# Kernel tuning notes

Hardware: AMD Instinct MI355X
Metric: run time of the kernel (lower is better)

The kernel has to match this reference:

```python
import jax, jax.numpy as jnp
import numpy as np

HEADS = 16
D_MODEL = 1024
GROUP = 4
SEQ = 2048
HEAD_DIM = D_MODEL // HEADS          # 64
KV_HEADS = HEADS // GROUP            # 4


def rope_tables(head_dim, seq_len, base=10000.0):
    # NOTE: faithful to source: exp = -2*arange(0,d,2)/d  (steps of 2 -> base^{-4j/d})
    exp = -2.0 * jnp.arange(0, head_dim, 2, dtype=jnp.float32) / head_dim
    thetas = jnp.power(base, exp)                       # [d/2]
    m = jnp.arange(seq_len, dtype=jnp.float32)          # [S]
    freq = jnp.outer(m, thetas)                         # [S, d/2]
    return jnp.cos(freq), jnp.sin(freq)


def apply_rope(x, cos, sin):
    # x: [B,S,H,D]; complex rotation on consecutive pairs
    B, S, H, D = x.shape
    xr = x.reshape(B, S, H, D // 2, 2)
    x0, x1 = xr[..., 0], xr[..., 1]
    c = cos[None, :S, None, :]
    s = sin[None, :S, None, :]
    out = jnp.stack([x0 * c - x1 * s, x0 * s + x1 * c], axis=-1)
    return out.reshape(B, S, H, D)


def setup_inputs() -> dict:
    key = jax.random.key(0)
    ks = jax.random.split(key, 8)
    B = 1
    q = jax.random.normal(ks[0], (B, SEQ, D_MODEL), dtype=jnp.float32)
    k = jax.random.normal(ks[1], (B, SEQ, D_MODEL), dtype=jnp.float32)
    v = jax.random.normal(ks[2], (B, SEQ, D_MODEL), dtype=jnp.float32)
    mask = jnp.tril(jnp.ones((SEQ, SEQ), dtype=jnp.int32))[None]  # causal [B,S,S]
    sc = 0.02
    Wq = jax.random.normal(ks[3], (D_MODEL, D_MODEL), dtype=jnp.float32) * sc
    Wk = jax.random.normal(ks[4], (D_MODEL, D_MODEL // GROUP), dtype=jnp.float32) * sc
    Wv = jax.random.normal(ks[5], (D_MODEL, D_MODEL // GROUP), dtype=jnp.float32) * sc
    Wo = jax.random.normal(ks[6], (D_MODEL, D_MODEL), dtype=jnp.float32) * sc
    bq = jnp.zeros((D_MODEL,), jnp.float32)
    bk = jnp.zeros((D_MODEL // GROUP,), jnp.float32)
    bv = jnp.zeros((D_MODEL // GROUP,), jnp.float32)
    bo = jnp.zeros((D_MODEL,), jnp.float32)
    return {"q": q, "k": k, "v": v, "mask": mask, "Wq": Wq, "bq": bq,
            "Wk": Wk, "bk": bk, "Wv": Wv, "bv": bv, "Wo": Wo, "bo": bo}


def reference(q, k, v, mask, Wq, bq, Wk, bk, Wv, bv, Wo, bo):
    B, S, _ = q.shape
    cos, sin = rope_tables(HEAD_DIM, S)
    qh = (q @ Wq + bq).reshape(B, S, HEADS, HEAD_DIM)
    kh = (k @ Wk + bk).reshape(B, S, KV_HEADS, HEAD_DIM)
    vh = (v @ Wv + bv).reshape(B, S, KV_HEADS, HEAD_DIM)
    qh = apply_rope(qh, cos, sin)
    kh = apply_rope(kh, cos, sin)
    qh = qh.transpose(0, 2, 1, 3)                       # [B,H,S,D]
    kh = kh.transpose(0, 2, 1, 3)                       # [B,Hkv,S,D]
    vh = vh.transpose(0, 2, 1, 3)
    # torch .repeat tiles: query head j attends kv head j % KV_HEADS
    kh = jnp.tile(kh, (1, GROUP, 1, 1))                 # [B,H,S,D]
    vh = jnp.tile(vh, (1, GROUP, 1, 1))
    scores = jnp.einsum('bhqd,bhkd->bhqk', qh, kh) / jnp.sqrt(
        jnp.asarray(HEAD_DIM, dtype=qh.dtype))
    scores = jnp.where(mask[:, None, :, :] == 0, -jnp.inf, scores)
    attn = jax.nn.softmax(scores, axis=-1)
    out = jnp.einsum('bhqk,bhkd->bhqd', attn, vh)
    out = out.transpose(0, 2, 1, 3).reshape(B, S, D_MODEL)
    return out @ Wo + bo
```

## Files before the change

kernel.cpp:

```cpp
#include <hip/hip_runtime.h>
#include <hip/hip_bf16.h>
#include <math.h>


#define SEQ 2048
#define DM 1024
#define HD 64

using u16 = unsigned short;
typedef __attribute__((ext_vector_type(8))) short bf16x8;
typedef __attribute__((ext_vector_type(4))) float f32x4;

#define QSCALE 0.18033688011112042f

__device__ __forceinline__ u16 f2b(float f) {
    union { float f; unsigned int i; } v; v.f = f;
    unsigned int u = v.i;
    return (u16)((u + 0x7fffu + ((u >> 16) & 1u)) >> 16);
}
__device__ __forceinline__ u16 f2b_fast(float f) {
    union { float f; unsigned int i; } v; v.f = f;
    return (u16)((v.i + 0x8000u) >> 16);
}

__global__ __launch_bounds__(256) void prep_kernel(
    const float* __restrict__ qin, const float* __restrict__ kin, const float* __restrict__ vin,
    const float* __restrict__ Wq, const float* __restrict__ Wk,
    const float* __restrict__ Wv, const float* __restrict__ Wo,
    u16* __restrict__ Xq, u16* __restrict__ Xk, u16* __restrict__ Xv,
    u16* __restrict__ Wt, u16* __restrict__ wot)
{
    const int b = blockIdx.x;
    const int t = threadIdx.x;

    if (b < 640) {
        __shared__ short T[64][72];
        const float* W; u16* dst; int N, t0, rowoff;
        if (b < 256)      { W = Wq; dst = Wt;  N = 1024; t0 = b;       rowoff = 0; }
        else if (b < 320) { W = Wk; dst = Wt;  N = 256;  t0 = b - 256; rowoff = 1024; }
        else if (b < 384) { W = Wv; dst = Wt;  N = 256;  t0 = b - 320; rowoff = 1280; }
        else              { W = Wo; dst = wot; N = 1024; t0 = b - 384; rowoff = 0; }
        const int ntn = N >> 6;
        const int k0 = (t0 / ntn) * 64, n0 = (t0 % ntn) * 64;
        const int r = t >> 4, c4 = (t & 15) * 4;
        #pragma unroll
        for (int rr = 0; rr < 4; ++rr) {
            const int k = r + rr * 16;
            float4 w4 = *reinterpret_cast<const float4*>(W + (size_t)(k0 + k) * N + n0 + c4);
            T[c4 + 0][k] = (short)f2b(w4.x);
            T[c4 + 1][k] = (short)f2b(w4.y);
            T[c4 + 2][k] = (short)f2b(w4.z);
            T[c4 + 3][k] = (short)f2b(w4.w);
        }
        __syncthreads();
        const int n = t >> 2, ck = (t & 3) * 16;
        u16* dp = dst + (size_t)(rowoff + n0 + n) * DM + k0 + ck;
        *reinterpret_cast<bf16x8*>(dp)     = *reinterpret_cast<const bf16x8*>(&T[n][ck]);
        *reinterpret_cast<bf16x8*>(dp + 8) = *reinterpret_cast<const bf16x8*>(&T[n][ck + 8]);
    } else {
        const int idx = b - 640;
        const int which = idx >> 8;
        const int ib = idx & 255;
        const float* src = (which == 0) ? qin : (which == 1) ? kin : vin;
        u16* dst = (which == 0) ? Xq : (which == 1) ? Xk : Xv;
        const size_t base = (size_t)ib * 8192 + (size_t)t * 32;
        #pragma unroll
        for (int c = 0; c < 4; ++c) {
            float4 x0 = *reinterpret_cast<const float4*>(src + base + c * 8);
            float4 x1 = *reinterpret_cast<const float4*>(src + base + c * 8 + 4);
            bf16x8 o;
            o[0] = (short)f2b(x0.x); o[1] = (short)f2b(x0.y);
            o[2] = (short)f2b(x0.z); o[3] = (short)f2b(x0.w);
            o[4] = (short)f2b(x1.x); o[5] = (short)f2b(x1.y);
            o[6] = (short)f2b(x1.z); o[7] = (short)f2b(x1.w);
            *reinterpret_cast<bf16x8*>(dst + base + c * 8) = o;
        }
    }
}

__global__ __launch_bounds__(256) void proj_mfma(
    const u16* __restrict__ Xq, const u16* __restrict__ Xk, const u16* __restrict__ Xv,
    const u16* __restrict__ Wt,
    const float* __restrict__ bq, const float* __restrict__ bk, const float* __restrict__ bv,
    u16* __restrict__ Qr, u16* __restrict__ Kr, u16* __restrict__ Vrt)
{
    const int n0 = blockIdx.x * 64, m0 = blockIdx.y * 64;
    const int zone = (n0 < 1024) ? 0 : (n0 < 1280) ? 1 : 2;
    const u16* __restrict__ Az = (zone == 0) ? Xq : (zone == 1) ? Xk : Xv;

    __shared__ short As[64][72];
    __shared__ short Bs[64][72];

    const int t = threadIdx.x;
    const int w = t >> 6, lane = t & 63, lm = lane & 15, quad = lane >> 4;
    const int sr = t >> 2, sc = (t & 3) * 16;

    f32x4 acc[4] = { {0,0,0,0}, {0,0,0,0}, {0,0,0,0}, {0,0,0,0} };

    for (int k0 = 0; k0 < DM; k0 += 64) {
        const u16* ap = Az + (size_t)(m0 + sr) * DM + k0 + sc;
        *reinterpret_cast<bf16x8*>(&As[sr][sc])     = *reinterpret_cast<const bf16x8*>(ap);
        *reinterpret_cast<bf16x8*>(&As[sr][sc + 8]) = *reinterpret_cast<const bf16x8*>(ap + 8);
        const u16* bp = Wt + (size_t)(n0 + sr) * DM + k0 + sc;
        *reinterpret_cast<bf16x8*>(&Bs[sr][sc])     = *reinterpret_cast<const bf16x8*>(bp);
        *reinterpret_cast<bf16x8*>(&Bs[sr][sc + 8]) = *reinterpret_cast<const bf16x8*>(bp + 8);
        __syncthreads();
        bf16x8 af0 = *reinterpret_cast<const bf16x8*>(&As[16 * w + lm][quad * 8]);
        bf16x8 af1 = *reinterpret_cast<const bf16x8*>(&As[16 * w + lm][32 + quad * 8]);
        #pragma unroll
        for (int nb = 0; nb < 4; ++nb) {
            bf16x8 b0 = *reinterpret_cast<const bf16x8*>(&Bs[16 * nb + lm][quad * 8]);
            bf16x8 b1 = *reinterpret_cast<const bf16x8*>(&Bs[16 * nb + lm][32 + quad * 8]);
            acc[nb] = __builtin_amdgcn_mfma_f32_16x16x32_bf16(af0, b0, acc[nb], 0, 0, 0);
            acc[nb] = __builtin_amdgcn_mfma_f32_16x16x32_bf16(af1, b1, acc[nb], 0, 0, 0);
        }
        __syncthreads();
    }

    const float* __restrict__ bias = (zone == 0) ? bq : (zone == 1) ? bk : bv;
    const int nbase = (zone == 0) ? n0 : (zone == 1) ? (n0 - 1024) : (n0 - 1280);
    const int head = nbase >> 6;
    #pragma unroll
    for (int nb = 0; nb < 4; ++nb) {
        const int d = 16 * nb + lm;
        const float bvv = bias[nbase + d];
        float vals[4];
        #pragma unroll
        for (int r = 0; r < 4; ++r) vals[r] = acc[nb][r] + bvv;
        if (zone != 2) {
            const int pi = d >> 1;
            const float theta = exp2f(-0.8304820237f * (float)pi);
            const bool odd = (lm & 1);
            const float sca = (zone == 0) ? QSCALE : 1.0f;
            #pragma unroll
            for (int r = 0; r < 4; ++r) {
                const int m = m0 + 16 * w + quad * 4 + r;
                float sn, cs;
                sincosf((float)m * theta, &sn, &cs);
                float x  = vals[r];
                float xp = __shfl_xor(x, 1);
                vals[r] = (odd ? (xp * sn + x * cs) : (x * cs - xp * sn)) * sca;
            }
            u16* op = (zone == 0 ? Qr : Kr) + (size_t)head * SEQ * HD;
            #pragma unroll
            for (int r = 0; r < 4; ++r) {
                const int m = m0 + 16 * w + quad * 4 + r;
                op[(size_t)m * HD + d] = f2b(vals[r]);
            }
        } else {
            u16 pk[4];
            #pragma unroll
            for (int r = 0; r < 4; ++r) pk[r] = f2b(vals[r]);
            u16* vp = Vrt + ((size_t)head * HD + d) * SEQ + m0 + 16 * w + quad * 4;
            *reinterpret_cast<uint2*>(vp) = *reinterpret_cast<uint2*>(pk);
        }
    }
}

__global__ __launch_bounds__(256) void attn_mfma(
    const u16* __restrict__ Qr, const u16* __restrict__ Kr, const u16* __restrict__ Vrt,
    u16* __restrict__ AO)
{
    const int h  = blockIdx.x;
    const int qy = blockIdx.y;
    const int qt = (qy < 16) ? (2 * qy) : (63 - 2 * qy);
    const int kvh = h & 3;

    __shared__ short Qs[64][72];
    __shared__ short Ks[2][64][72];
    __shared__ short Vt[64][136];
    __shared__ short Ps[64][136];
    __shared__ float Lred[4][64];

    const int t = threadIdx.x;
    const int w = t >> 6, lane = t & 63, lm = lane & 15, quad = lane >> 4;
    const int sr = t >> 2, sc = (t & 3) * 16;
    const int colb = (sc >> 4) * 32;

    {
        const u16* qp = Qr + ((size_t)h * SEQ + qt * 64 + sr) * HD + sc;
        *reinterpret_cast<bf16x8*>(&Qs[sr][sc])     = *reinterpret_cast<const bf16x8*>(qp);
        *reinterpret_cast<bf16x8*>(&Qs[sr][sc + 8]) = *reinterpret_cast<const bf16x8*>(qp + 8);
    }
    __syncthreads();
    bf16x8 bq[4][2];
    #pragma unroll
    for (int nb = 0; nb < 4; ++nb) {
        bq[nb][0] = *reinterpret_cast<const bf16x8*>(&Qs[16 * nb + lm][quad * 8]);
        bq[nb][1] = *reinterpret_cast<const bf16x8*>(&Qs[16 * nb + lm][32 + quad * 8]);
    }

    f32x4 O[4][4];
    #pragma unroll
    for (int i = 0; i < 4; ++i)
        #pragma unroll
        for (int j = 0; j < 4; ++j) O[i][j] = (f32x4){0.f, 0.f, 0.f, 0.f};
    float lp[4] = { 0.f, 0.f, 0.f, 0.f };

    const int ntile = qt + 1;
    const u16* kbase = Kr  + ((size_t)kvh * SEQ + sr) * HD + sc;
    const u16* vbase = Vrt + ((size_t)kvh * HD  + sr) * SEQ + sc;

    for (int u = 0; u < ntile; u += 2) {
        const bool has1 = (u + 1 < ntile);
        {
            const u16* kp0 = kbase + (size_t)u * 64 * HD;
            *reinterpret_cast<bf16x8*>(&Ks[0][sr][sc])     = *reinterpret_cast<const bf16x8*>(kp0);
            *reinterpret_cast<bf16x8*>(&Ks[0][sr][sc + 8]) = *reinterpret_cast<const bf16x8*>(kp0 + 8);
            const u16* vp0 = vbase + (size_t)u * 64;
            *reinterpret_cast<bf16x8*>(&Vt[sr][colb])      = *reinterpret_cast<const bf16x8*>(vp0);
            *reinterpret_cast<bf16x8*>(&Vt[sr][colb + 8])  = *reinterpret_cast<const bf16x8*>(vp0 + 8);
            if (has1) {
                const u16* kp1 = kbase + (size_t)(u + 1) * 64 * HD;
                *reinterpret_cast<bf16x8*>(&Ks[1][sr][sc])     = *reinterpret_cast<const bf16x8*>(kp1);
                *reinterpret_cast<bf16x8*>(&Ks[1][sr][sc + 8]) = *reinterpret_cast<const bf16x8*>(kp1 + 8);
                const u16* vp1 = vbase + (size_t)(u + 1) * 64;
                *reinterpret_cast<bf16x8*>(&Vt[sr][colb + 16]) = *reinterpret_cast<const bf16x8*>(vp1);
                *reinterpret_cast<bf16x8*>(&Vt[sr][colb + 24]) = *reinterpret_cast<const bf16x8*>(vp1 + 8);
            } else {
                bf16x8 z = {0,0,0,0,0,0,0,0};
                *reinterpret_cast<bf16x8*>(&Vt[sr][colb + 16]) = z;
                *reinterpret_cast<bf16x8*>(&Vt[sr][colb + 24]) = z;
            }
        }
        __syncthreads();

        #pragma unroll
        for (int tp = 0; tp < 2; ++tp) {
            const int kt = u + tp;
            if (tp == 1 && !has1) {
                const uint2 z2 = make_uint2(0u, 0u);
                #pragma unroll
                for (int nb = 0; nb < 4; ++nb)
                    *reinterpret_cast<uint2*>(&Ps[16 * nb + lm][w * 32 + 16 + quad * 4]) = z2;
                continue;
            }
            const bf16x8 ak0 = *reinterpret_cast<const bf16x8*>(&Ks[tp][16 * w + lm][quad * 8]);
            const bf16x8 ak1 = *reinterpret_cast<const bf16x8*>(&Ks[tp][16 * w + lm][32 + quad * 8]);
            const bool diag = (kt == qt);
            #pragma unroll
            for (int nb = 0; nb < 4; ++nb) {
                f32x4 ss = { 0.f, 0.f, 0.f, 0.f };
                ss = __builtin_amdgcn_mfma_f32_16x16x32_bf16(ak0, bq[nb][0], ss, 0, 0, 0);
                ss = __builtin_amdgcn_mfma_f32_16x16x32_bf16(ak1, bq[nb][1], ss, 0, 0, 0);
                u16 pk[4];
                #pragma unroll
                for (int r = 0; r < 4; ++r) {
                    float sv = ss[r];
                    if (diag && (16 * w + quad * 4 + r > 16 * nb + lm)) sv = -INFINITY;
                    float e = __builtin_amdgcn_exp2f(fminf(sv, 126.f));
                    lp[nb] += e;
                    pk[r] = f2b_fast(e);
                }
                *reinterpret_cast<uint2*>(&Ps[16 * nb + lm][w * 32 + tp * 16 + quad * 4]) =
                    *reinterpret_cast<uint2*>(pk);
            }
        }

        #pragma unroll
        for (int db = 0; db < 4; ++db) {
            const bf16x8 av = *reinterpret_cast<const bf16x8*>(&Vt[16 * db + lm][w * 32 + quad * 8]);
            #pragma unroll
            for (int nb = 0; nb < 4; ++nb) {
                const bf16x8 bp = *reinterpret_cast<const bf16x8*>(&Ps[16 * nb + lm][w * 32 + quad * 8]);
                O[db][nb] = __builtin_amdgcn_mfma_f32_16x16x32_bf16(av, bp, O[db][nb], 0, 0, 0);
            }
        }
        __syncthreads();
    }

    #pragma unroll
    for (int nb = 0; nb < 4; ++nb) {
        lp[nb] += __shfl_xor(lp[nb], 16);
        lp[nb] += __shfl_xor(lp[nb], 32);
    }
    if (quad == 0) {
        #pragma unroll
        for (int nb = 0; nb < 4; ++nb) Lred[w][16 * nb + lm] = lp[nb];
    }

    float* Sf = reinterpret_cast<float*>(&Ps[0][0]);
    #pragma unroll
    for (int ph = 0; ph < 4; ++ph) {
        __syncthreads();
        if (w == ph) {
            #pragma unroll
            for (int db = 0; db < 4; ++db)
                #pragma unroll
                for (int nb = 0; nb < 4; ++nb)
                    #pragma unroll
                    for (int r = 0; r < 4; ++r) {
                        const int d = 16 * db + quad * 4 + r, q = 16 * nb + lm;
                        const float v = O[db][nb][r];
                        Sf[q * 68 + d] = (ph == 0) ? v : (Sf[q * 68 + d] + v);
                    }
        }
    }
    __syncthreads();

    {
        const int q = t >> 2, dc = (t & 3) * 16;
        const float linv = 1.0f / (Lred[0][q] + Lred[1][q] + Lred[2][q] + Lred[3][q]);
        u16 pk[16];
        #pragma unroll
        for (int j = 0; j < 16; ++j)
            pk[j] = f2b(Sf[q * 68 + dc + j] * linv);
        u16* op = AO + (size_t)(qt * 64 + q) * DM + h * HD + dc;
        *reinterpret_cast<bf16x8*>(op)     = *reinterpret_cast<const bf16x8*>(pk);
        *reinterpret_cast<bf16x8*>(op + 8) = *reinterpret_cast<const bf16x8*>(pk + 8);
    }
}

__global__ __launch_bounds__(256) void oproj_mfma(
    const u16* __restrict__ AO, const u16* __restrict__ wot,
    const float* __restrict__ bo, float* __restrict__ out)
{
    __shared__ short As[64][72];
    __shared__ short Bs[64][72];
    const int t = threadIdx.x;
    const int w = t >> 6, lane = t & 63, lm = lane & 15, quad = lane >> 4;
    const int m0 = blockIdx.y * 64, n0 = blockIdx.x * 64;
    const int sr = t >> 2, sc = (t & 3) * 16;

    f32x4 acc[4] = { {0,0,0,0}, {0,0,0,0}, {0,0,0,0}, {0,0,0,0} };

    for (int k0 = 0; k0 < DM; k0 += 64) {
        const u16* ap = AO + (size_t)(m0 + sr) * DM + k0 + sc;
        *reinterpret_cast<bf16x8*>(&As[sr][sc])     = *reinterpret_cast<const bf16x8*>(ap);
        *reinterpret_cast<bf16x8*>(&As[sr][sc + 8]) = *reinterpret_cast<const bf16x8*>(ap + 8);
        const u16* bp = wot + (size_t)(n0 + sr) * DM + k0 + sc;
        *reinterpret_cast<bf16x8*>(&Bs[sr][sc])     = *reinterpret_cast<const bf16x8*>(bp);
        *reinterpret_cast<bf16x8*>(&Bs[sr][sc + 8]) = *reinterpret_cast<const bf16x8*>(bp + 8);
        __syncthreads();
        bf16x8 af0 = *reinterpret_cast<const bf16x8*>(&As[16 * w + lm][quad * 8]);
        bf16x8 af1 = *reinterpret_cast<const bf16x8*>(&As[16 * w + lm][32 + quad * 8]);
        #pragma unroll
        for (int nb = 0; nb < 4; ++nb) {
            bf16x8 b0 = *reinterpret_cast<const bf16x8*>(&Bs[16 * nb + lm][quad * 8]);
            bf16x8 b1 = *reinterpret_cast<const bf16x8*>(&Bs[16 * nb + lm][32 + quad * 8]);
            acc[nb] = __builtin_amdgcn_mfma_f32_16x16x32_bf16(af0, b0, acc[nb], 0, 0, 0);
            acc[nb] = __builtin_amdgcn_mfma_f32_16x16x32_bf16(af1, b1, acc[nb], 0, 0, 0);
        }
        __syncthreads();
    }

    #pragma unroll
    for (int nb = 0; nb < 4; ++nb) {
        const int dl = 16 * nb + lm;
        const float bv = bo[n0 + dl];
        #pragma unroll
        for (int r = 0; r < 4; ++r) {
            const int m = m0 + 16 * w + quad * 4 + r;
            out[(size_t)m * DM + n0 + dl] = acc[nb][r] + bv;
        }
    }
}

extern "C" void kernel_launch(void* const* d_in, const int* in_sizes, int n_in,
                              void* d_out, int out_size, void* d_ws, size_t ws_size,
                              hipStream_t stream)
{
    const float* q  = (const float*)d_in[0];
    const float* k  = (const float*)d_in[1];
    const float* v  = (const float*)d_in[2];
    const float* Wq = (const float*)d_in[4];
    const float* bq = (const float*)d_in[5];
    const float* Wk = (const float*)d_in[6];
    const float* bk = (const float*)d_in[7];
    const float* Wv = (const float*)d_in[8];
    const float* bv = (const float*)d_in[9];
    const float* Wo = (const float*)d_in[10];
    const float* bo = (const float*)d_in[11];
    float* out = (float*)d_out;

    u16* Xq  = (u16*)d_ws;
    u16* Xk  = Xq  + (size_t)SEQ * DM;
    u16* Xv  = Xk  + (size_t)SEQ * DM;
    u16* Wt  = Xv  + (size_t)SEQ * DM;
    u16* wot = Wt  + (size_t)1536 * 1024;
    u16* Qr  = wot + (size_t)1024 * 1024;
    u16* Kr  = Qr  + (size_t)16 * SEQ * HD;
    u16* Vrt = Kr  + (size_t)4 * SEQ * HD;
    u16* AO  = Vrt + (size_t)4 * SEQ * HD;

    hipLaunchKernelGGL(prep_kernel, dim3(1408), dim3(256), 0, stream,
                       q, k, v, Wq, Wk, Wv, Wo, Xq, Xk, Xv, Wt, wot);
    hipLaunchKernelGGL(proj_mfma, dim3(24, 32), dim3(256), 0, stream,
                       Xq, Xk, Xv, Wt, bq, bk, bv, Qr, Kr, Vrt);
    hipLaunchKernelGGL(attn_mfma, dim3(16, 32), dim3(256), 0, stream,
                       Qr, Kr, Vrt, AO);
    hipLaunchKernelGGL(oproj_mfma, dim3(16, 32), dim3(256), 0, stream,
                       AO, wot, bo, out);
}
```

Baseline: 184.0 us.

## Replace LDS-tiled GEMMs and attention with register-direct per-wave MFMA loads

```diff
diff --git a/kernel.cpp b/kernel.cpp
--- a/kernel.cpp
+++ b/kernel.cpp
@@ -84,77 +84,92 @@
     const float* __restrict__ bq, const float* __restrict__ bk, const float* __restrict__ bv,
     u16* __restrict__ Qr, u16* __restrict__ Kr, u16* __restrict__ Vrt)
 {
-    const int n0 = blockIdx.x * 64, m0 = blockIdx.y * 64;
+    const int t = threadIdx.x;
+    const int w = t >> 6, lane = t & 63, lm = lane & 15, quad = lane >> 4;
+    const int n0 = blockIdx.x * 64 + (w & 1) * 32;
+    const int m0 = blockIdx.y * 64 + (w >> 1) * 32;
     const int zone = (n0 < 1024) ? 0 : (n0 < 1280) ? 1 : 2;
     const u16* __restrict__ Az = (zone == 0) ? Xq : (zone == 1) ? Xk : Xv;
 
-    __shared__ short As[64][72];
-    __shared__ short Bs[64][72];
-
-    const int t = threadIdx.x;
-    const int w = t >> 6, lane = t & 63, lm = lane & 15, quad = lane >> 4;
-    const int sr = t >> 2, sc = (t & 3) * 16;
-
-    f32x4 acc[4] = { {0,0,0,0}, {0,0,0,0}, {0,0,0,0}, {0,0,0,0} };
-
-    for (int k0 = 0; k0 < DM; k0 += 64) {
-        const u16* ap = Az + (size_t)(m0 + sr) * DM + k0 + sc;
-        *reinterpret_cast<bf16x8*>(&As[sr][sc])     = *reinterpret_cast<const bf16x8*>(ap);
-        *reinterpret_cast<bf16x8*>(&As[sr][sc + 8]) = *reinterpret_cast<const bf16x8*>(ap + 8);
-        const u16* bp = Wt + (size_t)(n0 + sr) * DM + k0 + sc;
-        *reinterpret_cast<bf16x8*>(&Bs[sr][sc])     = *reinterpret_cast<const bf16x8*>(bp);
-        *reinterpret_cast<bf16x8*>(&Bs[sr][sc + 8]) = *reinterpret_cast<const bf16x8*>(bp + 8);
-        __syncthreads();
-        bf16x8 af0 = *reinterpret_cast<const bf16x8*>(&As[16 * w + lm][quad * 8]);
-        bf16x8 af1 = *reinterpret_cast<const bf16x8*>(&As[16 * w + lm][32 + quad * 8]);
-        #pragma unroll
-        for (int nb = 0; nb < 4; ++nb) {
-            bf16x8 b0 = *reinterpret_cast<const bf16x8*>(&Bs[16 * nb + lm][quad * 8]);
-            bf16x8 b1 = *reinterpret_cast<const bf16x8*>(&Bs[16 * nb + lm][32 + quad * 8]);
-            acc[nb] = __builtin_amdgcn_mfma_f32_16x16x32_bf16(af0, b0, acc[nb], 0, 0, 0);
-            acc[nb] = __builtin_amdgcn_mfma_f32_16x16x32_bf16(af1, b1, acc[nb], 0, 0, 0);
-        }
-        __syncthreads();
+    const u16* arow[2] = { Az + (size_t)(m0 + lm) * DM + quad * 8,
+                           Az + (size_t)(m0 + 16 + lm) * DM + quad * 8 };
+    const u16* brow[2] = { Wt + (size_t)(n0 + lm) * DM + quad * 8,
+                           Wt + (size_t)(n0 + 16 + lm) * DM + quad * 8 };
+
+    f32x4 acc[2][2];
+    #pragma unroll
+    for (int i = 0; i < 2; ++i)
+        #pragma unroll
+        for (int j = 0; j < 2; ++j) acc[i][j] = (f32x4){0.f, 0.f, 0.f, 0.f};
+
+    bf16x8 a0[2], b0[2], a1[2], b1[2];
+    #pragma unroll
+    for (int i = 0; i < 2; ++i) {
+        a0[i] = *reinterpret_cast<const bf16x8*>(arow[i]);
+        b0[i] = *reinterpret_cast<const bf16x8*>(brow[i]);
+    }
+    for (int k = 0; k < DM; k += 64) {
+        #pragma unroll
+        for (int i = 0; i < 2; ++i) {
+            a1[i] = *reinterpret_cast<const bf16x8*>(arow[i] + k + 32);
+            b1[i] = *reinterpret_cast<const bf16x8*>(brow[i] + k + 32);
+        }
+        #pragma unroll
+        for (int mi = 0; mi < 2; ++mi)
+            #pragma unroll
+            for (int ni = 0; ni < 2; ++ni)
+                acc[mi][ni] = __builtin_amdgcn_mfma_f32_16x16x32_bf16(a0[mi], b0[ni], acc[mi][ni], 0, 0, 0);
+        if (k + 64 < DM) {
+            #pragma unroll
+            for (int i = 0; i < 2; ++i) {
+                a0[i] = *reinterpret_cast<const bf16x8*>(arow[i] + k + 64);
+                b0[i] = *reinterpret_cast<const bf16x8*>(brow[i] + k + 64);
+            }
+        }
+        #pragma unroll
+        for (int mi = 0; mi < 2; ++mi)
+            #pragma unroll
+            for (int ni = 0; ni < 2; ++ni)
+                acc[mi][ni] = __builtin_amdgcn_mfma_f32_16x16x32_bf16(a1[mi], b1[ni], acc[mi][ni], 0, 0, 0);
     }
 
     const float* __restrict__ bias = (zone == 0) ? bq : (zone == 1) ? bk : bv;
-    const int nbase = (zone == 0) ? n0 : (zone == 1) ? (n0 - 1024) : (n0 - 1280);
-    const int head = nbase >> 6;
-    #pragma unroll
-    for (int nb = 0; nb < 4; ++nb) {
-        const int d = 16 * nb + lm;
-        const float bvv = bias[nbase + d];
-        float vals[4];
-        #pragma unroll
-        for (int r = 0; r < 4; ++r) vals[r] = acc[nb][r] + bvv;
-        if (zone != 2) {
-            const int pi = d >> 1;
-            const float theta = exp2f(-0.8304820237f * (float)pi);
-            const bool odd = (lm & 1);
-            const float sca = (zone == 0) ? QSCALE : 1.0f;
-            #pragma unroll
-            for (int r = 0; r < 4; ++r) {
-                const int m = m0 + 16 * w + quad * 4 + r;
-                float sn, cs;
-                sincosf((float)m * theta, &sn, &cs);
-                float x  = vals[r];
-                float xp = __shfl_xor(x, 1);
-                vals[r] = (odd ? (xp * sn + x * cs) : (x * cs - xp * sn)) * sca;
-            }
-            u16* op = (zone == 0 ? Qr : Kr) + (size_t)head * SEQ * HD;
-            #pragma unroll
-            for (int r = 0; r < 4; ++r) {
-                const int m = m0 + 16 * w + quad * 4 + r;
-                op[(size_t)m * HD + d] = f2b(vals[r]);
-            }
-        } else {
-            u16 pk[4];
-            #pragma unroll
-            for (int r = 0; r < 4; ++r) pk[r] = f2b(vals[r]);
-            u16* vp = Vrt + ((size_t)head * HD + d) * SEQ + m0 + 16 * w + quad * 4;
-            *reinterpret_cast<uint2*>(vp) = *reinterpret_cast<uint2*>(pk);
-        }
-    }
+    const int zoff = (zone == 0) ? 0 : (zone == 1) ? 1024 : 1280;
+    #pragma unroll
+    for (int mi = 0; mi < 2; ++mi)
+        #pragma unroll
+        for (int ni = 0; ni < 2; ++ni) {
+            const int zc = (n0 - zoff) + ni * 16 + lm;
+            const int head = zc >> 6, d = zc & 63;
+            const float bvv = bias[zc];
+            float vals[4];
+            #pragma unroll
+            for (int r = 0; r < 4; ++r) vals[r] = acc[mi][ni][r] + bvv;
+            if (zone != 2) {
+                const int pi = d >> 1;
+                const float theta = exp2f(-0.8304820237f * (float)pi);
+                const bool odd = (lm & 1);
+                const float sca = (zone == 0) ? QSCALE : 1.0f;
+                u16* op = (zone == 0 ? Qr : Kr) + (size_t)head * SEQ * HD;
+                #pragma unroll
+                for (int r = 0; r < 4; ++r) {
+                    const int m = m0 + mi * 16 + quad * 4 + r;
+                    float sn, cs;
+                    sincosf((float)m * theta, &sn, &cs);
+                    float x  = vals[r];
+                    float xp = __shfl_xor(x, 1);
+                    float o  = (odd ? (xp * sn + x * cs) : (x * cs - xp * sn)) * sca;
+                    op[(size_t)m * HD + d] = f2b(o);
+                }
+            } else {
+                u16 pk[4];
+                #pragma unroll
+                for (int r = 0; r < 4; ++r) pk[r] = f2b(vals[r]);
+                const int m = m0 + mi * 16 + quad * 4;
+                u16* vp = Vrt + ((size_t)head * HD + d) * SEQ + m;
+                *reinterpret_cast<uint2*>(vp) = *reinterpret_cast<uint2*>(pk);
+            }
+        }
 }
 
 __global__ __launch_bounds__(256) void attn_mfma(
@@ -166,148 +181,83 @@
     const int qt = (qy < 16) ? (2 * qy) : (63 - 2 * qy);
     const int kvh = h & 3;
 
-    __shared__ short Qs[64][72];
-    __shared__ short Ks[2][64][72];
-    __shared__ short Vt[64][136];
-    __shared__ short Ps[64][136];
-    __shared__ float Lred[4][64];
+    __shared__ u16 Ps[4][16][76];
 
     const int t = threadIdx.x;
     const int w = t >> 6, lane = t & 63, lm = lane & 15, quad = lane >> 4;
-    const int sr = t >> 2, sc = (t & 3) * 16;
-    const int colb = (sc >> 4) * 32;
-
-    {
-        const u16* qp = Qr + ((size_t)h * SEQ + qt * 64 + sr) * HD + sc;
-        *reinterpret_cast<bf16x8*>(&Qs[sr][sc])     = *reinterpret_cast<const bf16x8*>(qp);
-        *reinterpret_cast<bf16x8*>(&Qs[sr][sc + 8]) = *reinterpret_cast<const bf16x8*>(qp + 8);
-    }
-    __syncthreads();
-    bf16x8 bq[4][2];
-    #pragma unroll
-    for (int nb = 0; nb < 4; ++nb) {
-        bq[nb][0] = *reinterpret_cast<const bf16x8*>(&Qs[16 * nb + lm][quad * 8]);
-        bq[nb][1] = *reinterpret_cast<const bf16x8*>(&Qs[16 * nb + lm][32 + quad * 8]);
-    }
-
-    f32x4 O[4][4];
-    #pragma unroll
-    for (int i = 0; i < 4; ++i)
-        #pragma unroll
-        for (int j = 0; j < 4; ++j) O[i][j] = (f32x4){0.f, 0.f, 0.f, 0.f};
+
+    const u16* qp = Qr + ((size_t)h * SEQ + qt * 64 + 16 * w + lm) * HD + quad * 8;
+    const bf16x8 aq0 = *reinterpret_cast<const bf16x8*>(qp);
+    const bf16x8 aq1 = *reinterpret_cast<const bf16x8*>(qp + 32);
+
+    const u16* krow = Kr  + ((size_t)kvh * SEQ + lm) * HD + quad * 8;
+    const u16* vrow = Vrt + ((size_t)kvh * HD + lm) * SEQ + quad * 8;
+
+    f32x4 O[4] = { {0,0,0,0}, {0,0,0,0}, {0,0,0,0}, {0,0,0,0} };
     float lp[4] = { 0.f, 0.f, 0.f, 0.f };
 
-    const int ntile = qt + 1;
-    const u16* kbase = Kr  + ((size_t)kvh * SEQ + sr) * HD + sc;
-    const u16* vbase = Vrt + ((size_t)kvh * HD  + sr) * SEQ + sc;
-
-    for (int u = 0; u < ntile; u += 2) {
-        const bool has1 = (u + 1 < ntile);
-        {
-            const u16* kp0 = kbase + (size_t)u * 64 * HD;
-            *reinterpret_cast<bf16x8*>(&Ks[0][sr][sc])     = *reinterpret_cast<const bf16x8*>(kp0);
-            *reinterpret_cast<bf16x8*>(&Ks[0][sr][sc + 8]) = *reinterpret_cast<const bf16x8*>(kp0 + 8);
-            const u16* vp0 = vbase + (size_t)u * 64;
-            *reinterpret_cast<bf16x8*>(&Vt[sr][colb])      = *reinterpret_cast<const bf16x8*>(vp0);
-            *reinterpret_cast<bf16x8*>(&Vt[sr][colb + 8])  = *reinterpret_cast<const bf16x8*>(vp0 + 8);
-            if (has1) {
-                const u16* kp1 = kbase + (size_t)(u + 1) * 64 * HD;
-                *reinterpret_cast<bf16x8*>(&Ks[1][sr][sc])     = *reinterpret_cast<const bf16x8*>(kp1);
-                *reinterpret_cast<bf16x8*>(&Ks[1][sr][sc + 8]) = *reinterpret_cast<const bf16x8*>(kp1 + 8);
-                const u16* vp1 = vbase + (size_t)(u + 1) * 64;
-                *reinterpret_cast<bf16x8*>(&Vt[sr][colb + 16]) = *reinterpret_cast<const bf16x8*>(vp1);
-                *reinterpret_cast<bf16x8*>(&Vt[sr][colb + 24]) = *reinterpret_cast<const bf16x8*>(vp1 + 8);
-            } else {
-                bf16x8 z = {0,0,0,0,0,0,0,0};
-                *reinterpret_cast<bf16x8*>(&Vt[sr][colb + 16]) = z;
-                *reinterpret_cast<bf16x8*>(&Vt[sr][colb + 24]) = z;
-            }
-        }
-        __syncthreads();
-
-        #pragma unroll
-        for (int tp = 0; tp < 2; ++tp) {
-            const int kt = u + tp;
-            if (tp == 1 && !has1) {
-                const uint2 z2 = make_uint2(0u, 0u);
+    u16* ps = &Ps[w][0][0];
+
+    for (int kt = 0; kt <= qt; ++kt) {
+        const int kb = kt * 64;
+        bf16x8 kb0[4], kb1[4], vb0[4], vb1[4];
+        #pragma unroll
+        for (int nb = 0; nb < 4; ++nb) {
+            const u16* kp = krow + (size_t)(kb + 16 * nb) * HD;
+            kb0[nb] = *reinterpret_cast<const bf16x8*>(kp);
+            kb1[nb] = *reinterpret_cast<const bf16x8*>(kp + 32);
+        }
+        #pragma unroll
+        for (int db = 0; db < 4; ++db) {
+            const u16* vp = vrow + (size_t)(16 * db) * SEQ + kb;
+            vb0[db] = *reinterpret_cast<const bf16x8*>(vp);
+            vb1[db] = *reinterpret_cast<const bf16x8*>(vp + 32);
+        }
+
+        f32x4 s[4];
+        #pragma unroll
+        for (int nb = 0; nb < 4; ++nb) {
+            f32x4 zz = { 0.f, 0.f, 0.f, 0.f };
+            zz = __builtin_amdgcn_mfma_f32_16x16x32_bf16(aq0, kb0[nb], zz, 0, 0, 0);
+            s[nb] = __builtin_amdgcn_mfma_f32_16x16x32_bf16(aq1, kb1[nb], zz, 0, 0, 0);
+        }
+
+        if (kt == qt) {
+            #pragma unroll
+            for (int nb = 0; nb < 4; ++nb)
                 #pragma unroll
-                for (int nb = 0; nb < 4; ++nb)
-                    *reinterpret_cast<uint2*>(&Ps[16 * nb + lm][w * 32 + 16 + quad * 4]) = z2;
-                continue;
-            }
-            const bf16x8 ak0 = *reinterpret_cast<const bf16x8*>(&Ks[tp][16 * w + lm][quad * 8]);
-            const bf16x8 ak1 = *reinterpret_cast<const bf16x8*>(&Ks[tp][16 * w + lm][32 + quad * 8]);
-            const bool diag = (kt == qt);
-            #pragma unroll
-            for (int nb = 0; nb < 4; ++nb) {
-                f32x4 ss = { 0.f, 0.f, 0.f, 0.f };
-                ss = __builtin_amdgcn_mfma_f32_16x16x32_bf16(ak0, bq[nb][0], ss, 0, 0, 0);
-                ss = __builtin_amdgcn_mfma_f32_16x16x32_bf16(ak1, bq[nb][1], ss, 0, 0, 0);
-                u16 pk[4];
-                #pragma unroll
-                for (int r = 0; r < 4; ++r) {
-                    float sv = ss[r];
-                    if (diag && (16 * w + quad * 4 + r > 16 * nb + lm)) sv = -INFINITY;
-                    float e = __builtin_amdgcn_exp2f(fminf(sv, 126.f));
-                    lp[nb] += e;
-                    pk[r] = f2b_fast(e);
-                }
-                *reinterpret_cast<uint2*>(&Ps[16 * nb + lm][w * 32 + tp * 16 + quad * 4]) =
-                    *reinterpret_cast<uint2*>(pk);
-            }
-        }
-
+                for (int r = 0; r < 4; ++r)
+                    if (16 * nb + lm > 16 * w + quad * 4 + r) s[nb][r] = -INFINITY;
+        }
+
+        #pragma unroll
+        for (int nb = 0; nb < 4; ++nb)
+            #pragma unroll
+            for (int r = 0; r < 4; ++r) {
+                float e = __builtin_amdgcn_exp2f(fminf(s[nb][r], 126.f));
+                lp[r] += e;
+                ps[(quad * 4 + r) * 76 + 16 * nb + lm] = f2b_fast(e);
+            }
+
+        const bf16x8 ap0 = *reinterpret_cast<const bf16x8*>(&ps[lm * 76 + quad * 8]);
+        const bf16x8 ap1 = *reinterpret_cast<const bf16x8*>(&ps[lm * 76 + 32 + quad * 8]);
         #pragma unroll
         for (int db = 0; db < 4; ++db) {
-            const bf16x8 av = *reinterpret_cast<const bf16x8*>(&Vt[16 * db + lm][w * 32 + quad * 8]);
-            #pragma unroll
-            for (int nb = 0; nb < 4; ++nb) {
-                const bf16x8 bp = *reinterpret_cast<const bf16x8*>(&Ps[16 * nb + lm][w * 32 + quad * 8]);
-                O[db][nb] = __builtin_amdgcn_mfma_f32_16x16x32_bf16(av, bp, O[db][nb], 0, 0, 0);
-            }
-        }
-        __syncthreads();
-    }
-
-    #pragma unroll
-    for (int nb = 0; nb < 4; ++nb) {
-        lp[nb] += __shfl_xor(lp[nb], 16);
-        lp[nb] += __shfl_xor(lp[nb], 32);
-    }
-    if (quad == 0) {
-        #pragma unroll
-        for (int nb = 0; nb < 4; ++nb) Lred[w][16 * nb + lm] = lp[nb];
-    }
-
-    float* Sf = reinterpret_cast<float*>(&Ps[0][0]);
-    #pragma unroll
-    for (int ph = 0; ph < 4; ++ph) {
-        __syncthreads();
-        if (w == ph) {
-            #pragma unroll
-            for (int db = 0; db < 4; ++db)
-                #pragma unroll
-                for (int nb = 0; nb < 4; ++nb)
-                    #pragma unroll
-                    for (int r = 0; r < 4; ++r) {
-                        const int d = 16 * db + quad * 4 + r, q = 16 * nb + lm;
-                        const float v = O[db][nb][r];
-                        Sf[q * 68 + d] = (ph == 0) ? v : (Sf[q * 68 + d] + v);
-                    }
-        }
-    }
-    __syncthreads();
-
-    {
-        const int q = t >> 2, dc = (t & 3) * 16;
-        const float linv = 1.0f / (Lred[0][q] + Lred[1][q] + Lred[2][q] + Lred[3][q]);
-        u16 pk[16];
-        #pragma unroll
-        for (int j = 0; j < 16; ++j)
-            pk[j] = f2b(Sf[q * 68 + dc + j] * linv);
-        u16* op = AO + (size_t)(qt * 64 + q) * DM + h * HD + dc;
-        *reinterpret_cast<bf16x8*>(op)     = *reinterpret_cast<const bf16x8*>(pk);
-        *reinterpret_cast<bf16x8*>(op + 8) = *reinterpret_cast<const bf16x8*>(pk + 8);
+            O[db] = __builtin_amdgcn_mfma_f32_16x16x32_bf16(ap0, vb0[db], O[db], 0, 0, 0);
+            O[db] = __builtin_amdgcn_mfma_f32_16x16x32_bf16(ap1, vb1[db], O[db], 0, 0, 0);
+        }
+    }
+
+    #pragma unroll
+    for (int r = 0; r < 4; ++r) {
+        #pragma unroll
+        for (int off = 1; off < 16; off <<= 1)
+            lp[r] += __shfl_xor(lp[r], off);
+        const float inv = 1.0f / lp[r];
+        const size_t row = (size_t)(qt * 64 + 16 * w + quad * 4 + r) * DM + (size_t)h * HD;
+        #pragma unroll
+        for (int db = 0; db < 4; ++db)
+            AO[row + 16 * db + lm] = f2b(O[db][r] * inv);
     }
 }
 
@@ -315,45 +265,65 @@
     const u16* __restrict__ AO, const u16* __restrict__ wot,
     const float* __restrict__ bo, float* __restrict__ out)
 {
-    __shared__ short As[64][72];
-    __shared__ short Bs[64][72];
     const int t = threadIdx.x;
     const int w = t >> 6, lane = t & 63, lm = lane & 15, quad = lane >> 4;
-    const int m0 = blockIdx.y * 64, n0 = blockIdx.x * 64;
-    const int sr = t >> 2, sc = (t & 3) * 16;
-
-    f32x4 acc[4] = { {0,0,0,0}, {0,0,0,0}, {0,0,0,0}, {0,0,0,0} };
-
-    for (int k0 = 0; k0 < DM; k0 += 64) {
-        const u16* ap = AO + (size_t)(m0 + sr) * DM + k0 + sc;
-        *reinterpret_cast<bf16x8*>(&As[sr][sc])     = *reinterpret_cast<const bf16x8*>(ap);
-        *reinterpret_cast<bf16x8*>(&As[sr][sc + 8]) = *reinterpret_cast<const bf16x8*>(ap + 8);
-        const u16* bp = wot + (size_t)(n0 + sr) * DM + k0 + sc;
-        *reinterpret_cast<bf16x8*>(&Bs[sr][sc])     = *reinterpret_cast<const bf16x8*>(bp);
-        *reinterpret_cast<bf16x8*>(&Bs[sr][sc + 8]) = *reinterpret_cast<const bf16x8*>(bp + 8);
-        __syncthreads();
-        bf16x8 af0 = *reinterpret_cast<const bf16x8*>(&As[16 * w + lm][quad * 8]);
-        bf16x8 af1 = *reinterpret_cast<const bf16x8*>(&As[16 * w + lm][32 + quad * 8]);
-        #pragma unroll
-        for (int nb = 0; nb < 4; ++nb) {
-            bf16x8 b0 = *reinterpret_cast<const bf16x8*>(&Bs[16 * nb + lm][quad * 8]);
-            bf16x8 b1 = *reinterpret_cast<const bf16x8*>(&Bs[16 * nb + lm][32 + quad * 8]);
-            acc[nb] = __builtin_amdgcn_mfma_f32_16x16x32_bf16(af0, b0, acc[nb], 0, 0, 0);
-            acc[nb] = __builtin_amdgcn_mfma_f32_16x16x32_bf16(af1, b1, acc[nb], 0, 0, 0);
-        }
-        __syncthreads();
-    }
-
-    #pragma unroll
-    for (int nb = 0; nb < 4; ++nb) {
-        const int dl = 16 * nb + lm;
-        const float bv = bo[n0 + dl];
-        #pragma unroll
-        for (int r = 0; r < 4; ++r) {
-            const int m = m0 + 16 * w + quad * 4 + r;
-            out[(size_t)m * DM + n0 + dl] = acc[nb][r] + bv;
-        }
-    }
+    const int n0 = blockIdx.x * 64 + (w & 1) * 32;
+    const int m0 = blockIdx.y * 64 + (w >> 1) * 32;
+
+    const u16* arow[2] = { AO  + (size_t)(m0 + lm) * DM + quad * 8,
+                           AO  + (size_t)(m0 + 16 + lm) * DM + quad * 8 };
+    const u16* brow[2] = { wot + (size_t)(n0 + lm) * DM + quad * 8,
+                           wot + (size_t)(n0 + 16 + lm) * DM + quad * 8 };
+
+    f32x4 acc[2][2];
+    #pragma unroll
+    for (int i = 0; i < 2; ++i)
+        #pragma unroll
+        for (int j = 0; j < 2; ++j) acc[i][j] = (f32x4){0.f, 0.f, 0.f, 0.f};
+
+    bf16x8 a0[2], b0[2], a1[2], b1[2];
+    #pragma unroll
+    for (int i = 0; i < 2; ++i) {
+        a0[i] = *reinterpret_cast<const bf16x8*>(arow[i]);
+        b0[i] = *reinterpret_cast<const bf16x8*>(brow[i]);
+    }
+    for (int k = 0; k < DM; k += 64) {
+        #pragma unroll
+        for (int i = 0; i < 2; ++i) {
+            a1[i] = *reinterpret_cast<const bf16x8*>(arow[i] + k + 32);
+            b1[i] = *reinterpret_cast<const bf16x8*>(brow[i] + k + 32);
+        }
+        #pragma unroll
+        for (int mi = 0; mi < 2; ++mi)
+            #pragma unroll
+            for (int ni = 0; ni < 2; ++ni)
+                acc[mi][ni] = __builtin_amdgcn_mfma_f32_16x16x32_bf16(a0[mi], b0[ni], acc[mi][ni], 0, 0, 0);
+        if (k + 64 < DM) {
+            #pragma unroll
+            for (int i = 0; i < 2; ++i) {
+                a0[i] = *reinterpret_cast<const bf16x8*>(arow[i] + k + 64);
+                b0[i] = *reinterpret_cast<const bf16x8*>(brow[i] + k + 64);
+            }
+        }
+        #pragma unroll
+        for (int mi = 0; mi < 2; ++mi)
+            #pragma unroll
+            for (int ni = 0; ni < 2; ++ni)
+                acc[mi][ni] = __builtin_amdgcn_mfma_f32_16x16x32_bf16(a1[mi], b1[ni], acc[mi][ni], 0, 0, 0);
+    }
+
+    #pragma unroll
+    for (int mi = 0; mi < 2; ++mi)
+        #pragma unroll
+        for (int ni = 0; ni < 2; ++ni) {
+            const int ncol = n0 + ni * 16 + lm;
+            const float bvv = bo[ncol];
+            #pragma unroll
+            for (int r = 0; r < 4; ++r) {
+                const int m = m0 + mi * 16 + quad * 4 + r;
+                out[(size_t)m * DM + ncol] = acc[mi][ni][r] + bvv;
+            }
+        }
 }
 
 extern "C" void kernel_launch(void* const* d_in, const int* in_sizes, int n_in,
```

Measured after the change: 248.7 us. 35.2% more time.
